# Optimization experiments

Hardware: AMD Instinct MI355X
Metric: run time of the kernel (lower is better)

Reference implementation:

```python
import jax, jax.numpy as jnp
import numpy as np

N_NODES = 50000
N_EDGES = 800000
N_GRAPHS = 512
HID = 128
RBF_DIM = 32
N_LAYERS = 6
CUTOFF = 4.0
GAMMA = 0.5 / (CUTOFF / RBF_DIM) ** 2  # 32.0
CENTERS = jnp.linspace(0.0, CUTOFF, RBF_DIM)


def ssp(x):
    return jax.nn.softplus(x) - 0.5


def setup_inputs() -> dict:
    key = jax.random.key(0)
    ks = jax.random.split(key, 24)
    s = 0.05
    inp = {
        "z": jax.random.randint(ks[0], (N_NODES,), 0, 11),
        "pos": jax.random.normal(ks[1], (N_NODES, 3), jnp.float32) * 3.0,
        "edge_index": jax.random.randint(ks[2], (2, N_EDGES), 0, N_NODES),
        "batch": jnp.sort(jax.random.randint(ks[3], (N_NODES,), 0, N_GRAPHS)),
        "embed": jax.random.normal(ks[4], (11, HID), jnp.float32) * s,
        # per-layer stacked params for 6 SchNetConv layers
        "fw1": jax.random.normal(ks[5], (N_LAYERS, RBF_DIM, HID), jnp.float32) * s,
        "fb1": jnp.zeros((N_LAYERS, HID), jnp.float32),
        "fw2": jax.random.normal(ks[6], (N_LAYERS, HID, HID), jnp.float32) * s,
        "fb2": jnp.zeros((N_LAYERS, HID), jnp.float32),
        "uw1": jax.random.normal(ks[7], (N_LAYERS, HID, HID), jnp.float32) * s,
        "ub1": jnp.zeros((N_LAYERS, HID), jnp.float32),
        "uw2": jax.random.normal(ks[8], (N_LAYERS, HID, HID), jnp.float32) * s,
        "ub2": jnp.zeros((N_LAYERS, HID), jnp.float32),
        # output block
        "ow1": jax.random.normal(ks[9], (HID, HID), jnp.float32) * s,
        "ob1": jnp.zeros((HID,), jnp.float32),
        "ow2": jax.random.normal(ks[10], (HID, HID), jnp.float32) * s,
        "ob2": jnp.zeros((HID,), jnp.float32),
        "ow3": jax.random.normal(ks[11], (HID, 1), jnp.float32) * s,
        "ob3": jnp.zeros((1,), jnp.float32),
    }
    return inp


def _forward(z, pos, edge_index, batch, embed, fw1, fb1, fw2, fb2,
             uw1, ub1, uw2, ub2, ow1, ob1, ow2, ob2, ow3, ob3):
    i, j = edge_index[0], edge_index[1]
    h = embed[z]                                         # [N, H]
    # geometry is fixed across layers (pos never updated)
    rel = pos[i] - pos[j]                                # [E, 3]
    dist = jnp.linalg.norm(rel, axis=-1, keepdims=True)  # [E, 1]
    rbf = jnp.exp(-GAMMA * (dist - CENTERS[None, :]) ** 2)  # [E, RBF]
    deg = jax.ops.segment_sum(jnp.ones((i.shape[0],), h.dtype), i,
                              num_segments=N_NODES)
    inv_deg = 1.0 / jnp.maximum(deg, 1.0)                # [N]
    for l in range(N_LAYERS):
        W = ssp(rbf @ fw1[l] + fb1[l]) @ fw2[l] + fb2[l]  # [E, H]
        m_ij = h[j] * W                                   # [E, H]
        aggr = jax.ops.segment_sum(m_ij, i, num_segments=N_NODES)
        aggr = aggr * inv_deg[:, None]
        h = ssp(aggr @ uw1[l] + ub1[l]) @ uw2[l] + ub2[l]
    # output block: per-atom MLP -> scalar, then sum per graph
    e = ssp(h @ ow1 + ob1)
    e = ssp(e @ ow2 + ob2)
    e_atom = (e @ ow3 + ob3)[:, 0]                       # [N]
    energy = jax.ops.segment_sum(e_atom, batch, num_segments=N_GRAPHS)
    return energy                                        # [N_GRAPHS]


def reference(z, pos, edge_index, batch, embed, fw1, fb1, fw2, fb2,
              uw1, ub1, uw2, ub2, ow1, ob1, ow2, ob2, ow3, ob3):
    return _forward(z, pos, edge_index, batch, embed, fw1, fb1, fw2, fb2,
                    uw1, ub1, uw2, ub2, ow1, ob1, ow2, ob2, ow3, ob3)
```

## Files before the change

### kernel.cpp

```cpp
#include <hip/hip_runtime.h>
#include <math.h>

#define HID 128
#define RBF 32
#define NL 6
#define BINS 4096
#define DMAXF 5.0f
#define INV_STEP (4096.0f / 5.0f)
#define GAMMAF 32.0f
#define CSPACE (4.0f / 31.0f)
#define TM 32

typedef _Float16 half8v __attribute__((ext_vector_type(8)));
typedef _Float16 half4v __attribute__((ext_vector_type(4)));
typedef float f32x4 __attribute__((ext_vector_type(4)));

__device__ __forceinline__ float sspf(float x) {
    return fmaxf(x, 0.0f) + __logf(1.0f + __expf(-fabsf(x))) - 0.5f;
}


#define SB 256
__global__ void k_scan1(const int* __restrict__ counts, int* __restrict__ pre,
                        int* __restrict__ bsums, int n) {
    __shared__ int s[SB];
    int tid = threadIdx.x;
    int g = blockIdx.x * SB + tid;
    int v = (g < n) ? counts[g] : 0;
    s[tid] = v;
    __syncthreads();
    for (int off = 1; off < SB; off <<= 1) {
        int t = (tid >= off) ? s[tid - off] : 0;
        __syncthreads();
        s[tid] += t;
        __syncthreads();
    }
    if (g < n) pre[g] = s[tid] - v;
    if (tid == SB - 1) bsums[blockIdx.x] = s[tid];
}

__global__ void k_scan2(int* __restrict__ bsums, int nb) {
    __shared__ int s[1024];
    int tid = threadIdx.x;
    int v = (tid < nb) ? bsums[tid] : 0;
    s[tid] = v;
    __syncthreads();
    for (int off = 1; off < 1024; off <<= 1) {
        int t = (tid >= off) ? s[tid - off] : 0;
        __syncthreads();
        s[tid] += t;
        __syncthreads();
    }
    if (tid < nb) bsums[tid] = s[tid] - v;
}

__global__ void k_scan3(const int* __restrict__ pre, const int* __restrict__ bsums,
                        const int* __restrict__ counts, int* __restrict__ row_ofs,
                        int* __restrict__ curF, int* __restrict__ curB,
                        float* __restrict__ invdeg, int n) {
    int g = blockIdx.x * SB + threadIdx.x;
    if (g >= n) return;
    int r = pre[g] + bsums[g >> 8];
    row_ofs[g] = r;
    curF[g] = r;
    curB[g] = r + counts[g];
    invdeg[g] = 1.0f / fmaxf((float)counts[g], 1.0f);
    if (g == n - 1) row_ofs[n] = r + counts[g];
}

__global__ void k_scatter(const int* __restrict__ ei, const float* __restrict__ pos,
                          int* __restrict__ curF, int* __restrict__ curB,
                          unsigned int* __restrict__ epk, int E_) {
    int e = blockIdx.x * blockDim.x + threadIdx.x;
    if (e >= E_) return;
    int i = ei[e], j = ei[E_ + e];
    float dx = pos[3 * i]     - pos[3 * j];
    float dy = pos[3 * i + 1] - pos[3 * j + 1];
    float dz = pos[3 * i + 2] - pos[3 * j + 2];
    float d = sqrtf(dx * dx + dy * dy + dz * dz);
    float t = fminf(d, DMAXF) * INV_STEP;
    unsigned int b = (unsigned int)(t + 0.5f);
    int p;
    if (b == BINS) p = atomicAdd(&curF[i], 1);
    else           p = atomicSub(&curB[i], 1) - 1;
    epk[p] = (unsigned int)j | (b << 17);
}

__global__ void k_counthinit(const int* __restrict__ ei, int* __restrict__ counts, int E_,
                             const int* __restrict__ z, const float* __restrict__ embed,
                             _Float16* __restrict__ h, int total4, int A) {
    if ((int)blockIdx.x < A) {
        int e = blockIdx.x * blockDim.x + threadIdx.x;
        if (e < E_) atomicAdd(&counts[ei[e]], 1);
    } else {
        int idx = (blockIdx.x - A) * blockDim.x + threadIdx.x;
        if (idx >= total4) return;
        int node = idx >> 5, q = idx & 31;
        float4 v = ((const float4*)embed)[(size_t)z[node] * 32 + q];
        half4v o;
        o[0] = (_Float16)v.x; o[1] = (_Float16)v.y;
        o[2] = (_Float16)v.z; o[3] = (_Float16)v.w;
        *(half4v*)(h + (size_t)node * HID + q * 4) = o;
    }
}

__global__ void k_packall(const float* __restrict__ uw1, const float* __restrict__ uw2,
                          const float* __restrict__ fw2, const float* __restrict__ ow1,
                          const float* __restrict__ ow2, const float* __restrict__ fw1,
                          _Float16* __restrict__ uw1b, _Float16* __restrict__ uw2b,
                          _Float16* __restrict__ w2tf, _Float16* __restrict__ ow1b,
                          _Float16* __restrict__ ow2b, _Float16* __restrict__ w1tf) {
    int y = blockIdx.y;
    int lane = threadIdx.x;
    int m = lane & 15, g = lane >> 4;
    if (y < 20) {
        const float* src;
        _Float16* dst;
        if (y < 6)       { src = uw1 + (size_t)y * 16384;        dst = uw1b + (size_t)y * 16384; }
        else if (y < 12) { src = uw2 + (size_t)(y - 6) * 16384;  dst = uw2b + (size_t)(y - 6) * 16384; }
        else if (y < 18) { src = fw2 + (size_t)(y - 12) * 16384; dst = w2tf + (size_t)(y - 12) * 16384; }
        else if (y == 18){ src = ow1;                            dst = ow1b; }
        else             { src = ow2;                            dst = ow2b; }
        int b = blockIdx.x;
        int kt = b >> 3, nt = b & 7;
        _Float16* d = dst + ((size_t)b * 64 + lane) * 8;
#pragma unroll
        for (int j = 0; j < 8; ++j)
            d[j] = (_Float16)src[(32 * kt + 8 * g + j) * 128 + 16 * nt + m];
    } else {
        int l = y - 20;
        int nt = blockIdx.x;
        if (nt >= 8) return;
        const float* src = fw1 + (size_t)l * RBF * HID;
        _Float16* d = w1tf + (size_t)l * RBF * HID + ((size_t)nt * 64 + lane) * 8;
#pragma unroll
        for (int j = 0; j < 8; ++j)
            d[j] = (_Float16)src[(8 * g + j) * 128 + 16 * nt + m];
    }
}

__device__ __forceinline__ void gemm64(const _Float16 (*A)[136], const _Float16* __restrict__ Wf,
                                       int lane, int c0, f32x4 acc[4][2]) {
    const int m = lane & 15, g = lane >> 4;
#pragma unroll
    for (int kt = 0; kt < 4; ++kt) {
        half8v a[4];
#pragma unroll
        for (int rt = 0; rt < 4; ++rt)
            a[rt] = *(const half8v*)&A[16 * rt + m][kt * 32 + g * 8];
#pragma unroll
        for (int t = 0; t < 2; ++t) {
            int nt = (c0 >> 4) + t;
            half8v b = *(const half8v*)(Wf + (((size_t)kt * 8 + nt) * 64 + lane) * 8);
#pragma unroll
            for (int rt = 0; rt < 4; ++rt)
                acc[rt][t] = __builtin_amdgcn_mfma_f32_16x16x32_f16(a[rt], b, acc[rt][t], 0, 0, 0);
        }
    }
}

__device__ __forceinline__ void gemm32(const _Float16 (*A)[136], const _Float16* __restrict__ Wf,
                                       int lane, int c0, f32x4 acc[2][2]) {
    const int m = lane & 15, g = lane >> 4;
#pragma unroll
    for (int kt = 0; kt < 4; ++kt) {
        half8v a[2];
#pragma unroll
        for (int rt = 0; rt < 2; ++rt)
            a[rt] = *(const half8v*)&A[16 * rt + m][kt * 32 + g * 8];
#pragma unroll
        for (int t = 0; t < 2; ++t) {
            int nt = (c0 >> 4) + t;
            half8v b = *(const half8v*)(Wf + (((size_t)kt * 8 + nt) * 64 + lane) * 8);
#pragma unroll
            for (int rt = 0; rt < 2; ++rt)
                acc[rt][t] = __builtin_amdgcn_mfma_f32_16x16x32_f16(a[rt], b, acc[rt][t], 0, 0, 0);
        }
    }
}

template <bool SSP>
__device__ __forceinline__ void epi64(_Float16 (*dst)[136], const float* __restrict__ bias,
                                      int lane, int c0, const f32x4 acc[4][2]) {
    const int m = lane & 15, g = lane >> 4;
    float bc0 = bias[c0 + m], bc1 = bias[c0 + 16 + m];
#pragma unroll
    for (int rt = 0; rt < 4; ++rt)
#pragma unroll
        for (int t = 0; t < 2; ++t) {
            int col = c0 + 16 * t + m;
            float bc = t ? bc1 : bc0;
#pragma unroll
            for (int reg = 0; reg < 4; ++reg) {
                float v = acc[rt][t][reg] + bc;
                dst[16 * rt + 4 * g + reg][col] = (_Float16)(SSP ? sspf(v) : v);
            }
        }
}

template <bool SSP>
__device__ __forceinline__ void epi32(_Float16 (*dst)[136], const float* __restrict__ bias,
                                      int lane, int c0, const f32x4 acc[2][2]) {
    const int m = lane & 15, g = lane >> 4;
    float bc0 = bias[c0 + m], bc1 = bias[c0 + 16 + m];
#pragma unroll
    for (int rt = 0; rt < 2; ++rt)
#pragma unroll
        for (int t = 0; t < 2; ++t) {
            int col = c0 + 16 * t + m;
            float bc = t ? bc1 : bc0;
#pragma unroll
            for (int reg = 0; reg < 4; ++reg) {
                float v = acc[rt][t][reg] + bc;
                dst[16 * rt + 4 * g + reg][col] = (_Float16)(SSP ? sspf(v) : v);
            }
        }
}

__global__ __launch_bounds__(256) void k_tabmm(const _Float16* __restrict__ w1f,
                                               const float* __restrict__ fb1,
                                               const _Float16* __restrict__ w2f,
                                               const float* __restrict__ fb2,
                                               _Float16* __restrict__ tables) {
    __shared__ _Float16 R[64][40];
    __shared__ _Float16 T[64][136];
    const int tid = threadIdx.x;
    const int wave = tid >> 6, lane = tid & 63;
    const int m = lane & 15, g = lane >> 4;
    const int l = blockIdx.y;
    const int bin0 = blockIdx.x * 64;
    const int c0 = wave * 32;

    {
        int r = tid >> 2, cc0 = (tid & 3) * 8;
        float d = (float)(bin0 + r) * (DMAXF / (float)BINS);
#pragma unroll
        for (int j = 0; j < 8; ++j) {
            float dd = d - (float)(cc0 + j) * CSPACE;
            R[r][cc0 + j] = (_Float16)__expf(-GAMMAF * dd * dd);
        }
    }
    __syncthreads();

    f32x4 acc[4][2];
#pragma unroll
    for (int rt = 0; rt < 4; ++rt)
#pragma unroll
        for (int t = 0; t < 2; ++t) acc[rt][t] = (f32x4){0.f, 0.f, 0.f, 0.f};
    {
        half8v a[4];
#pragma unroll
        for (int rt = 0; rt < 4; ++rt)
            a[rt] = *(const half8v*)&R[16 * rt + m][g * 8];
#pragma unroll
        for (int t = 0; t < 2; ++t) {
            int nt = (c0 >> 4) + t;
            half8v b = *(const half8v*)(w1f + (size_t)l * RBF * HID + ((size_t)nt * 64 + lane) * 8);
#pragma unroll
            for (int rt = 0; rt < 4; ++rt)
                acc[rt][t] = __builtin_amdgcn_mfma_f32_16x16x32_f16(a[rt], b, acc[rt][t], 0, 0, 0);
        }
    }
    epi64<true>(T, fb1 + l * HID, lane, c0, acc);
    __syncthreads();

#pragma unroll
    for (int rt = 0; rt < 4; ++rt)
#pragma unroll
        for (int t = 0; t < 2; ++t) acc[rt][t] = (f32x4){0.f, 0.f, 0.f, 0.f};
    gemm64(T, w2f + (size_t)l * 16384, lane, c0, acc);
    __syncthreads();
    epi64<false>(T, fb2 + l * HID, lane, c0, acc);
    __syncthreads();
    _Float16* dst = tables + (size_t)l * (BINS + 1) * HID;
    for (int it = tid; it < 1024; it += 256) {
        int row = it >> 4, cc = (it & 15) * 8;
        int bin = bin0 + row;
        if (bin <= BINS)
            *(half8v*)(dst + (size_t)bin * HID + cc) = *(const half8v*)&T[row][cc];
    }
}

template <int FINAL>
__global__ __launch_bounds__(256) void k_layer(
        const int* __restrict__ row_ofs, const unsigned int* __restrict__ epk,
        const _Float16* __restrict__ h, const _Float16* __restrict__ table,
        const float* __restrict__ invdeg,
        const _Float16* __restrict__ W1f, const float* __restrict__ b1,
        const _Float16* __restrict__ W2f, const float* __restrict__ b2,
        _Float16* __restrict__ Y,
        const _Float16* __restrict__ OW1f, const float* __restrict__ ob1,
        const _Float16* __restrict__ OW2f, const float* __restrict__ ob2,
        const float* __restrict__ ow3, const float* __restrict__ ob3,
        const int* __restrict__ batch, float* __restrict__ out, int n) {
    __shared__ _Float16 U[TM][136];
    __shared__ _Float16 T[TM][136];
    const int tid = threadIdx.x;
    const int wave = tid >> 6, lane = tid & 63;
    const int quarter = lane >> 4, sub = lane & 15;
    const int row0 = blockIdx.x * TM;
    const int c0 = wave * 32;

    const _Float16* hB = h + 8 * sub;
    const _Float16* tB = table + 8 * sub;
    const half8v tcl = *(const half8v*)(tB + (size_t)BINS * HID);
    for (int idx = 0; idx < TM / 4; ++idx) {
        int r = (TM / 4) * wave + idx;
        int node = row0 + r;
        int beg = 0, end = 0;
        if (node < n) { beg = row_ofs[node]; end = row_ofs[node + 1]; }
        half8v accA, accB;
#pragma unroll
        for (int q = 0; q < 8; ++q) { accA[q] = (_Float16)0.f; accB[q] = (_Float16)0.f; }
        int k = beg + quarter;
        while (k + 4 < end) {
            unsigned int pkA = epk[k];
            unsigned int pkB = epk[k + 4];
            int jA = pkA & 0x1FFFF, bA = (int)(pkA >> 17);
            int jB = pkB & 0x1FFFF, bB = (int)(pkB >> 17);
            half8v hjA = *(const half8v*)(hB + (size_t)jA * HID);
            half8v hjB = *(const half8v*)(hB + (size_t)jB * HID);
            half8v twA, twB;
            if (bA == BINS) twA = tcl;
            else            twA = *(const half8v*)(tB + (size_t)bA * HID);
            if (bB == BINS) twB = tcl;
            else            twB = *(const half8v*)(tB + (size_t)bB * HID);
            accA += hjA * twA;
            accB += hjB * twB;
            k += 8;
        }
        if (k < end) {
            unsigned int pk = epk[k];
            int j = pk & 0x1FFFF, b = (int)(pk >> 17);
            half8v hj = *(const half8v*)(hB + (size_t)j * HID);
            half8v tw;
            if (b == BINS) tw = tcl;
            else           tw = *(const half8v*)(tB + (size_t)b * HID);
            accA += hj * tw;
        }
        accA += accB;
        int4 ai = *(int4*)&accA;
#pragma unroll
        for (int o = 32; o >= 16; o >>= 1) {
            int4 oi;
            oi.x = __shfl_xor(ai.x, o);
            oi.y = __shfl_xor(ai.y, o);
            oi.z = __shfl_xor(ai.z, o);
            oi.w = __shfl_xor(ai.w, o);
            half8v ov = *(half8v*)&oi;
            half8v av = *(half8v*)&ai;
            av += ov;
            ai = *(int4*)&av;
        }
        if (quarter == 0) {
            half8v av = *(half8v*)&ai;
            float s = (node < n) ? invdeg[node] : 0.f;
            half8v o;
#pragma unroll
            for (int q = 0; q < 8; ++q) o[q] = (_Float16)((float)av[q] * s);
            *(half8v*)&U[r][8 * sub] = o;
        }
    }
    __syncthreads();

    f32x4 acc[2][2];
#pragma unroll
    for (int rt = 0; rt < 2; ++rt)
#pragma unroll
        for (int t = 0; t < 2; ++t) acc[rt][t] = (f32x4){0.f, 0.f, 0.f, 0.f};
    gemm32(U, W1f, lane, c0, acc);
    epi32<true>(T, b1, lane, c0, acc);
    __syncthreads();

#pragma unroll
    for (int rt = 0; rt < 2; ++rt)
#pragma unroll
        for (int t = 0; t < 2; ++t) acc[rt][t] = (f32x4){0.f, 0.f, 0.f, 0.f};
    gemm32(T, W2f, lane, c0, acc);

    if (FINAL == 0) {
        epi32<false>(U, b2, lane, c0, acc);
        __syncthreads();
        for (int it = tid; it < TM * 16; it += 256) {
            int row = it >> 4, cc = (it & 15) * 8;
            int r = row0 + row;
            if (r < n)
                *(half8v*)(Y + (size_t)r * HID + cc) = *(const half8v*)&U[row][cc];
        }
    } else {
        epi32<false>(U, b2, lane, c0, acc);
        __syncthreads();
#pragma unroll
        for (int rt = 0; rt < 2; ++rt)
#pragma unroll
            for (int t = 0; t < 2; ++t) acc[rt][t] = (f32x4){0.f, 0.f, 0.f, 0.f};
        gemm32(U, OW1f, lane, c0, acc);
        epi32<true>(T, ob1, lane, c0, acc);
        __syncthreads();
#pragma unroll
        for (int rt = 0; rt < 2; ++rt)
#pragma unroll
            for (int t = 0; t < 2; ++t) acc[rt][t] = (f32x4){0.f, 0.f, 0.f, 0.f};
        gemm32(T, OW2f, lane, c0, acc);
        __shared__ float ea[4][TM];
        __shared__ float ev[TM];
        __shared__ int   bv[TM];
        const int m = lane & 15, g = lane >> 4;
        float bc0 = ob2[c0 + m], bc1 = ob2[c0 + 16 + m];
        float w0 = ow3[c0 + m], w1 = ow3[c0 + 16 + m];
#pragma unroll
        for (int rt = 0; rt < 2; ++rt) {
#pragma unroll
            for (int reg = 0; reg < 4; ++reg) {
                float p = sspf(acc[rt][0][reg] + bc0) * w0
                        + sspf(acc[rt][1][reg] + bc1) * w1;
                p += __shfl_xor(p, 1);
                p += __shfl_xor(p, 2);
                p += __shfl_xor(p, 4);
                p += __shfl_xor(p, 8);
                if (m == 0) ea[wave][16 * rt + 4 * g + reg] = p;
            }
        }
        __syncthreads();
        if (tid < TM) {
            int r = tid, row = row0 + r;
            float e = ea[0][r] + ea[1][r] + ea[2][r] + ea[3][r] + ob3[0];
            int bid = (row < n) ? batch[row] : -1;
            ev[r] = (row < n) ? e : 0.f;
            bv[r] = bid;
        }
        __syncthreads();
        if (tid < TM) {
            int r = tid, bid = bv[r];
            if (bid >= 0 && (r == 0 || bv[r - 1] != bid)) {
                float s = 0.f;
                for (int k2 = r; k2 < TM && bv[k2] == bid; ++k2) s += ev[k2];
                atomicAdd(&out[bid], s);
            }
        }
    }
}

extern "C" void kernel_launch(void* const* d_in, const int* in_sizes, int n_in,
                              void* d_out, int out_size, void* d_ws, size_t ws_size,
                              hipStream_t stream) {
    const int*   z     = (const int*)d_in[0];
    const float* pos   = (const float*)d_in[1];
    const int*   ei    = (const int*)d_in[2];
    const int*   batch = (const int*)d_in[3];
    const float* embed = (const float*)d_in[4];
    const float* fw1   = (const float*)d_in[5];
    const float* fb1   = (const float*)d_in[6];
    const float* fw2   = (const float*)d_in[7];
    const float* fb2   = (const float*)d_in[8];
    const float* uw1   = (const float*)d_in[9];
    const float* ub1   = (const float*)d_in[10];
    const float* uw2   = (const float*)d_in[11];
    const float* ub2   = (const float*)d_in[12];
    const float* ow1   = (const float*)d_in[13];
    const float* ob1   = (const float*)d_in[14];
    const float* ow2   = (const float*)d_in[15];
    const float* ob2   = (const float*)d_in[16];
    const float* ow3   = (const float*)d_in[17];
    const float* ob3   = (const float*)d_in[18];

    const int N = in_sizes[0];
    const int E = in_sizes[2] / 2;
    const int NB = (N + SB - 1) / SB;

    char* p = (char*)d_ws;
    auto alloc = [&](size_t bytes) {
        char* r = p;
        p += (bytes + 255) & ~(size_t)255;
        return r;
    };
    _Float16* h       = (_Float16*)alloc((size_t)(N + TM) * HID * 2);
    _Float16* h2      = (_Float16*)alloc((size_t)(N + TM) * HID * 2);
    unsigned int* epk = (unsigned int*)alloc((size_t)E * 4);
    int*      counts  = (int*)alloc((size_t)N * 4);
    int*      row_ofs = (int*)alloc((size_t)(N + 1) * 4);
    int*      curF    = (int*)alloc((size_t)N * 4);
    int*      curB    = (int*)alloc((size_t)N * 4);
    int*      pre     = (int*)alloc((size_t)N * 4);
    int*      bsums   = (int*)alloc((size_t)1024 * 4);
    float*    invdeg  = (float*)alloc((size_t)N * 4);
    _Float16* tab16   = (_Float16*)alloc((size_t)NL * (BINS + 1) * HID * 2);
    _Float16* w1tf    = (_Float16*)alloc((size_t)NL * RBF * HID * 2);
    _Float16* w2tf    = (_Float16*)alloc((size_t)NL * 16384 * 2);
    _Float16* uw1b    = (_Float16*)alloc((size_t)NL * 16384 * 2);
    _Float16* uw2b    = (_Float16*)alloc((size_t)NL * 16384 * 2);
    _Float16* ow1b    = (_Float16*)alloc((size_t)16384 * 2);
    _Float16* ow2b    = (_Float16*)alloc((size_t)16384 * 2);

    const int TB = 256;
    hipMemsetAsync(counts, 0, (size_t)N * 4, stream);
    hipMemsetAsync(d_out, 0, (size_t)out_size * sizeof(float), stream);

    int tot4 = N * 32;
    int A = (E + TB - 1) / TB;
    int B = (tot4 + TB - 1) / TB;
    k_counthinit<<<A + B, TB, 0, stream>>>(ei, counts, E, z, embed, h, tot4, A);
    k_packall<<<dim3(32, 26), 64, 0, stream>>>(uw1, uw2, fw2, ow1, ow2, fw1,
                                               uw1b, uw2b, w2tf, ow1b, ow2b, w1tf);
    k_scan1<<<NB, SB, 0, stream>>>(counts, pre, bsums, N);
    k_scan2<<<1, 1024, 0, stream>>>(bsums, NB);
    k_scan3<<<NB, SB, 0, stream>>>(pre, bsums, counts, row_ofs, curF, curB, invdeg, N);
    k_scatter<<<A, TB, 0, stream>>>(ei, pos, curF, curB, epk, E);
    k_tabmm<<<dim3((BINS + 1 + 63) / 64, NL), 256, 0, stream>>>(w1tf, fb1, w2tf, fb2, tab16);

    int mblocks = (N + TM - 1) / TM;

    _Float16* cur = h;
    _Float16* nxt = h2;
    for (int l = 0; l < NL - 1; ++l) {
        k_layer<0><<<mblocks, TB, 0, stream>>>(row_ofs, epk, cur,
                                               tab16 + (size_t)l * (BINS + 1) * HID, invdeg,
                                               uw1b + (size_t)l * 16384, ub1 + (size_t)l * HID,
                                               uw2b + (size_t)l * 16384, ub2 + (size_t)l * HID,
                                               nxt,
                                               nullptr, nullptr, nullptr, nullptr,
                                               nullptr, nullptr, nullptr, nullptr, N);
        _Float16* tmp = cur; cur = nxt; nxt = tmp;
    }
    k_layer<1><<<mblocks, TB, 0, stream>>>(row_ofs, epk, cur,
                                           tab16 + (size_t)(NL - 1) * (BINS + 1) * HID, invdeg,
                                           uw1b + (size_t)(NL - 1) * 16384, ub1 + (size_t)(NL - 1) * HID,
                                           uw2b + (size_t)(NL - 1) * 16384, ub2 + (size_t)(NL - 1) * HID,
                                           nullptr,
                                           ow1b, ob1, ow2b, ob2,
                                           ow3, ob3, batch, (float*)d_out, N);
}
```

Baseline: 458.7 us.

## Store node features as per-row int8 with scale to halve gather traffic

Node hidden states are now kept as 8-bit values with one float scale per node, in place of fp16. The embedding init and each layer's output write quantize to this format, and the edge gather dequantizes on the fly while accumulating in fp32. The goal is to halve the bytes moved by the random neighbor gathers that dominate the aggregation. In exchange it adds a scale load per edge, more unpack arithmetic, and doubles the register use of the accumulators, and the 8-bit quantization loses precision.

```diff
diff --git a/kernel.cpp b/kernel.cpp
--- a/kernel.cpp
+++ b/kernel.cpp
@@ -17,6 +17,20 @@
 
 __device__ __forceinline__ float sspf(float x) {
     return fmaxf(x, 0.0f) + __logf(1.0f + __expf(-fabsf(x))) - 0.5f;
+}
+
+__device__ __forceinline__ unsigned q1(float x, float inv) {
+    float f = fminf(fmaxf(x * inv + 128.5f, 0.0f), 255.0f);
+    return (unsigned)f;
+}
+
+__device__ __forceinline__ uint2 pack8(const float* v, float inv) {
+    unsigned r0 = 0, r1 = 0;
+#pragma unroll
+    for (int q = 0; q < 4; ++q) r0 |= q1(v[q], inv) << (8 * q);
+#pragma unroll
+    for (int q = 0; q < 4; ++q) r1 |= q1(v[4 + q], inv) << (8 * q);
+    return make_uint2(r0, r1);
 }
 
 
@@ -88,19 +102,28 @@
 
 __global__ void k_counthinit(const int* __restrict__ ei, int* __restrict__ counts, int E_,
                              const int* __restrict__ z, const float* __restrict__ embed,
-                             _Float16* __restrict__ h, int total4, int A) {
+                             unsigned char* __restrict__ hq, float* __restrict__ hs,
+                             int n, int A) {
     if ((int)blockIdx.x < A) {
         int e = blockIdx.x * blockDim.x + threadIdx.x;
         if (e < E_) atomicAdd(&counts[ei[e]], 1);
     } else {
-        int idx = (blockIdx.x - A) * blockDim.x + threadIdx.x;
-        if (idx >= total4) return;
-        int node = idx >> 5, q = idx & 31;
-        float4 v = ((const float4*)embed)[(size_t)z[node] * 32 + q];
-        half4v o;
-        o[0] = (_Float16)v.x; o[1] = (_Float16)v.y;
-        o[2] = (_Float16)v.z; o[3] = (_Float16)v.w;
-        *(half4v*)(h + (size_t)node * HID + q * 4) = o;
+        int t = (blockIdx.x - A) * blockDim.x + threadIdx.x;
+        int node = t >> 4, c8 = (t & 15) * 8;
+        if (node >= n) return;
+        const float* src = embed + (size_t)z[node] * HID + c8;
+        float4 a = *(const float4*)src;
+        float4 b = *(const float4*)(src + 4);
+        float v[8] = {a.x, a.y, a.z, a.w, b.x, b.y, b.z, b.w};
+        float mx = 0.f;
+#pragma unroll
+        for (int q = 0; q < 8; ++q) mx = fmaxf(mx, fabsf(v[q]));
+#pragma unroll
+        for (int o = 1; o < 16; o <<= 1) mx = fmaxf(mx, __shfl_xor(mx, o));
+        float s = mx * (1.0f / 127.0f);
+        float inv = (mx > 0.f) ? 127.0f / mx : 0.f;
+        *(uint2*)(hq + (size_t)node * HID + c8) = pack8(v, inv);
+        if ((t & 15) == 0) hs[node] = s;
     }
 }
 
@@ -284,11 +307,11 @@
 template <int FINAL>
 __global__ __launch_bounds__(256) void k_layer(
         const int* __restrict__ row_ofs, const unsigned int* __restrict__ epk,
-        const _Float16* __restrict__ h, const _Float16* __restrict__ table,
-        const float* __restrict__ invdeg,
+        const unsigned char* __restrict__ hq, const float* __restrict__ hs,
+        const _Float16* __restrict__ table, const float* __restrict__ invdeg,
         const _Float16* __restrict__ W1f, const float* __restrict__ b1,
         const _Float16* __restrict__ W2f, const float* __restrict__ b2,
-        _Float16* __restrict__ Y,
+        unsigned char* __restrict__ hqY, float* __restrict__ hsY,
         const _Float16* __restrict__ OW1f, const float* __restrict__ ob1,
         const _Float16* __restrict__ OW2f, const float* __restrict__ ob2,
         const float* __restrict__ ow3, const float* __restrict__ ob3,
@@ -301,7 +324,7 @@
     const int row0 = blockIdx.x * TM;
     const int c0 = wave * 32;
 
-    const _Float16* hB = h + 8 * sub;
+    const unsigned char* hB = hq + 8 * sub;
     const _Float16* tB = table + 8 * sub;
     const half8v tcl = *(const half8v*)(tB + (size_t)BINS * HID);
     for (int idx = 0; idx < TM / 4; ++idx) {
@@ -309,55 +332,59 @@
         int node = row0 + r;
         int beg = 0, end = 0;
         if (node < n) { beg = row_ofs[node]; end = row_ofs[node + 1]; }
-        half8v accA, accB;
-#pragma unroll
-        for (int q = 0; q < 8; ++q) { accA[q] = (_Float16)0.f; accB[q] = (_Float16)0.f; }
+        float accA[8], accB[8];
+#pragma unroll
+        for (int q = 0; q < 8; ++q) { accA[q] = 0.f; accB[q] = 0.f; }
         int k = beg + quarter;
         while (k + 4 < end) {
             unsigned int pkA = epk[k];
             unsigned int pkB = epk[k + 4];
             int jA = pkA & 0x1FFFF, bA = (int)(pkA >> 17);
             int jB = pkB & 0x1FFFF, bB = (int)(pkB >> 17);
-            half8v hjA = *(const half8v*)(hB + (size_t)jA * HID);
-            half8v hjB = *(const half8v*)(hB + (size_t)jB * HID);
+            uint2 haA = *(const uint2*)(hB + (size_t)jA * HID);
+            uint2 haB = *(const uint2*)(hB + (size_t)jB * HID);
+            float sA = hs[jA];
+            float sB = hs[jB];
             half8v twA, twB;
             if (bA == BINS) twA = tcl;
             else            twA = *(const half8v*)(tB + (size_t)bA * HID);
             if (bB == BINS) twB = tcl;
             else            twB = *(const half8v*)(tB + (size_t)bB * HID);
-            accA += hjA * twA;
-            accB += hjB * twB;
+#pragma unroll
+            for (int q = 0; q < 8; ++q) {
+                unsigned uA = (q < 4) ? ((haA.x >> (8 * q)) & 0xffu) : ((haA.y >> (8 * (q - 4))) & 0xffu);
+                unsigned uB = (q < 4) ? ((haB.x >> (8 * q)) & 0xffu) : ((haB.y >> (8 * (q - 4))) & 0xffu);
+                accA[q] += ((float)uA - 128.f) * ((float)twA[q] * sA);
+                accB[q] += ((float)uB - 128.f) * ((float)twB[q] * sB);
+            }
             k += 8;
         }
         if (k < end) {
             unsigned int pk = epk[k];
             int j = pk & 0x1FFFF, b = (int)(pk >> 17);
-            half8v hj = *(const half8v*)(hB + (size_t)j * HID);
+            uint2 ha = *(const uint2*)(hB + (size_t)j * HID);
+            float s = hs[j];
             half8v tw;
             if (b == BINS) tw = tcl;
             else           tw = *(const half8v*)(tB + (size_t)b * HID);
-            accA += hj * tw;
-        }
-        accA += accB;
-        int4 ai = *(int4*)&accA;
-#pragma unroll
-        for (int o = 32; o >= 16; o >>= 1) {
-            int4 oi;
-            oi.x = __shfl_xor(ai.x, o);
-            oi.y = __shfl_xor(ai.y, o);
-            oi.z = __shfl_xor(ai.z, o);
-            oi.w = __shfl_xor(ai.w, o);
-            half8v ov = *(half8v*)&oi;
-            half8v av = *(half8v*)&ai;
-            av += ov;
-            ai = *(int4*)&av;
+#pragma unroll
+            for (int q = 0; q < 8; ++q) {
+                unsigned u = (q < 4) ? ((ha.x >> (8 * q)) & 0xffu) : ((ha.y >> (8 * (q - 4))) & 0xffu);
+                accA[q] += ((float)u - 128.f) * ((float)tw[q] * s);
+            }
+        }
+#pragma unroll
+        for (int q = 0; q < 8; ++q) accA[q] += accB[q];
+#pragma unroll
+        for (int q = 0; q < 8; ++q) {
+            accA[q] += __shfl_xor(accA[q], 32);
+            accA[q] += __shfl_xor(accA[q], 16);
         }
         if (quarter == 0) {
-            half8v av = *(half8v*)&ai;
             float s = (node < n) ? invdeg[node] : 0.f;
             half8v o;
 #pragma unroll
-            for (int q = 0; q < 8; ++q) o[q] = (_Float16)((float)av[q] * s);
+            for (int q = 0; q < 8; ++q) o[q] = (_Float16)(accA[q] * s);
             *(half8v*)&U[r][8 * sub] = o;
         }
     }
@@ -384,8 +411,19 @@
         for (int it = tid; it < TM * 16; it += 256) {
             int row = it >> 4, cc = (it & 15) * 8;
             int r = row0 + row;
-            if (r < n)
-                *(half8v*)(Y + (size_t)r * HID + cc) = *(const half8v*)&U[row][cc];
+            half8v hv = *(const half8v*)&U[row][cc];
+            float v[8];
+            float mx = 0.f;
+#pragma unroll
+            for (int q = 0; q < 8; ++q) { v[q] = (float)hv[q]; mx = fmaxf(mx, fabsf(v[q])); }
+#pragma unroll
+            for (int o = 1; o < 16; o <<= 1) mx = fmaxf(mx, __shfl_xor(mx, o));
+            float s = mx * (1.0f / 127.0f);
+            float inv = (mx > 0.f) ? 127.0f / mx : 0.f;
+            if (r < n) {
+                *(uint2*)(hqY + (size_t)r * HID + cc) = pack8(v, inv);
+                if ((it & 15) == 0) hsY[r] = s;
+            }
         }
     } else {
         epi32<false>(U, b2, lane, c0, acc);
@@ -474,8 +512,10 @@
         p += (bytes + 255) & ~(size_t)255;
         return r;
     };
-    _Float16* h       = (_Float16*)alloc((size_t)(N + TM) * HID * 2);
-    _Float16* h2      = (_Float16*)alloc((size_t)(N + TM) * HID * 2);
+    unsigned char* hq1 = (unsigned char*)alloc((size_t)(N + TM) * HID);
+    unsigned char* hq2 = (unsigned char*)alloc((size_t)(N + TM) * HID);
+    float*    hs1     = (float*)alloc((size_t)(N + TM) * 4);
+    float*    hs2     = (float*)alloc((size_t)(N + TM) * 4);
     unsigned int* epk = (unsigned int*)alloc((size_t)E * 4);
     int*      counts  = (int*)alloc((size_t)N * 4);
     int*      row_ofs = (int*)alloc((size_t)(N + 1) * 4);
@@ -496,10 +536,9 @@
     hipMemsetAsync(counts, 0, (size_t)N * 4, stream);
     hipMemsetAsync(d_out, 0, (size_t)out_size * sizeof(float), stream);
 
-    int tot4 = N * 32;
     int A = (E + TB - 1) / TB;
-    int B = (tot4 + TB - 1) / TB;
-    k_counthinit<<<A + B, TB, 0, stream>>>(ei, counts, E, z, embed, h, tot4, A);
+    int B = (N * 16 + TB - 1) / TB;
+    k_counthinit<<<A + B, TB, 0, stream>>>(ei, counts, E, z, embed, hq1, hs1, N, A);
     k_packall<<<dim3(32, 26), 64, 0, stream>>>(uw1, uw2, fw2, ow1, ow2, fw1,
                                                uw1b, uw2b, w2tf, ow1b, ow2b, w1tf);
     k_scan1<<<NB, SB, 0, stream>>>(counts, pre, bsums, N);
@@ -510,23 +549,24 @@
 
     int mblocks = (N + TM - 1) / TM;
 
-    _Float16* cur = h;
-    _Float16* nxt = h2;
+    unsigned char* cq = hq1; float* cs = hs1;
+    unsigned char* nq = hq2; float* ns = hs2;
     for (int l = 0; l < NL - 1; ++l) {
-        k_layer<0><<<mblocks, TB, 0, stream>>>(row_ofs, epk, cur,
+        k_layer<0><<<mblocks, TB, 0, stream>>>(row_ofs, epk, cq, cs,
                                                tab16 + (size_t)l * (BINS + 1) * HID, invdeg,
                                                uw1b + (size_t)l * 16384, ub1 + (size_t)l * HID,
                                                uw2b + (size_t)l * 16384, ub2 + (size_t)l * HID,
-                                               nxt,
+                                               nq, ns,
                                                nullptr, nullptr, nullptr, nullptr,
                                                nullptr, nullptr, nullptr, nullptr, N);
-        _Float16* tmp = cur; cur = nxt; nxt = tmp;
-    }
-    k_layer<1><<<mblocks, TB, 0, stream>>>(row_ofs, epk, cur,
+        unsigned char* tq = cq; cq = nq; nq = tq;
+        float* ts = cs; cs = ns; ns = ts;
+    }
+    k_layer<1><<<mblocks, TB, 0, stream>>>(row_ofs, epk, cq, cs,
                                            tab16 + (size_t)(NL - 1) * (BINS + 1) * HID, invdeg,
                                            uw1b + (size_t)(NL - 1) * 16384, ub1 + (size_t)(NL - 1) * HID,
                                            uw2b + (size_t)(NL - 1) * 16384, ub2 + (size_t)(NL - 1) * HID,
-                                           nullptr,
+                                           nullptr, nullptr,
                                            ow1b, ob1, ow2b, ob2,
                                            ow3, ob3, batch, (float*)d_out, N);
 }
```

After: 576.5 us. 1.26x slower.
